# Performance work log

Hardware: AMD Instinct MI355X
Metric: run time of the kernel (lower is better)

Reference implementation:

```python
import jax, jax.numpy as jnp
import numpy as np

B, QS, KS, E, H = 2, 2048, 2048, 2048, 16
D = E // H  # head_dim = 128
EPS = 1e-6


def setup_inputs() -> dict:
    key = jax.random.key(0)
    ks = jax.random.split(key, 11)
    scale_in = 1.0 / np.sqrt(E)  # lecun_normal fan_in = E
    scale_out = 1.0 / np.sqrt(E)  # fan_in for out proj = H*D = E
    return {
        "q": jax.random.normal(ks[0], (B, QS, E), jnp.float32),
        "kv": jax.random.normal(ks[1], (B, KS, E), jnp.float32),
        "q_pos": jax.random.normal(ks[2], (B, QS, E), jnp.float32),
        "kv_pos": jax.random.normal(ks[3], (B, KS, E), jnp.float32),
        "mask": jax.random.bernoulli(ks[4], 0.5, (B, QS, KS)),
        "wq": jax.random.normal(ks[5], (E, H, D), jnp.float32) * scale_in,
        "wk": jax.random.normal(ks[6], (E, H, D), jnp.float32) * scale_in,
        "wv": jax.random.normal(ks[7], (E, H, D), jnp.float32) * scale_in,
        "q_ln_scale": jnp.ones((D,), jnp.float32),
        "k_ln_scale": jnp.ones((D,), jnp.float32),
        "wo": jax.random.normal(ks[8], (H, D, E), jnp.float32) * scale_out,
    }


def _layernorm_no_bias(x, scale):
    # flax LayerNorm over last axis, use_bias=False, epsilon=1e-6
    mu = jnp.mean(x, axis=-1, keepdims=True)
    var = jnp.mean(jnp.square(x - mu), axis=-1, keepdims=True)
    return (x - mu) * jax.lax.rsqrt(var + EPS) * scale


def reference(q, kv, q_pos, kv_pos, mask, wq, wk, wv, q_ln_scale, k_ln_scale, wo):
    dtype = q.dtype
    qi = q + q_pos          # [b, qs, e]
    ki = kv + kv_pos        # [b, ks, e]
    vi = kv
    # QKV projections (DenseGeneral, no bias) -> [b, s, h, d]
    qh = jnp.einsum('bqe,ehd->bqhd', qi, wq)
    kh = jnp.einsum('bke,ehd->bkhd', ki, wk)
    vh = jnp.einsum('bke,ehd->bkhd', vi, wv)
    # normalize_qk: LayerNorm (no bias) on query/key over head_dim
    qh = _layernorm_no_bias(qh, q_ln_scale)
    kh = _layernorm_no_bias(kh, k_ln_scale)
    # scaled dot-product with float32 logits
    qh = qh / jnp.sqrt(jnp.asarray(D, dtype))
    logits = jnp.einsum('bqhd,bkhd->bhqk', qh, kh,
                        preferred_element_type=jnp.float32)
    big_neg = jnp.finfo(jnp.float32).min
    logits = jnp.where(mask[:, None, :, :], logits, big_neg)
    attn = jax.nn.softmax(logits, axis=-1).astype(dtype)  # [b,h,q,k]
    out = jnp.einsum('bhqk,bkhd->bqhd', attn, vh)
    # output projection (DenseGeneral over (h,d), no bias)
    return jnp.einsum('bqhd,hde->bqe', out, wo)
```

## Files before the change

kernel.cpp:

```cpp
#include <hip/hip_runtime.h>
#include <hip/hip_bf16.h>


typedef __attribute__((ext_vector_type(8))) __bf16 bf16x8;
typedef __attribute__((ext_vector_type(4))) float f32x4;
typedef __attribute__((ext_vector_type(16))) float f32x16;
typedef __attribute__((ext_vector_type(8))) unsigned short ushort8;
typedef __attribute__((ext_vector_type(4))) unsigned short ushort4v;
typedef __attribute__((ext_vector_type(4))) unsigned uint4v;
typedef __attribute__((ext_vector_type(4))) float float4v;

#define MFMA16(a, b, c) __builtin_amdgcn_mfma_f32_16x16x32_bf16((a), (b), (c), 0, 0, 0)
#define MFMA32(a, b, c) __builtin_amdgcn_mfma_f32_32x32x16_bf16((a), (b), (c), 0, 0, 0)

__device__ __forceinline__ unsigned short f2bf(float f) {
  unsigned u = __builtin_bit_cast(unsigned, f);
  u += 0x7fffu + ((u >> 16) & 1u);
  return (unsigned short)(u >> 16);
}

__device__ __forceinline__ unsigned pkbf(float lo, float hi) {
  unsigned d;
  asm("v_cvt_pk_bf16_f32 %0, %1, %2" : "=v"(d) : "v"(lo), "v"(hi));
  return d;
}

__device__ __forceinline__ float max3f(float a, float b, float c) {
  float d;
  asm("v_max3_f32 %0, %1, %2, %3" : "=v"(d) : "v"(a), "v"(b), "v"(c));
  return d;
}

__device__ __forceinline__ float exp2a(float x) {
  float d;
  asm("v_exp_f32 %0, %1" : "=v"(d) : "v"(x));
  return d;
}

__device__ __forceinline__ void gload_lds16(const void* g, void* l) {
  __builtin_amdgcn_global_load_lds(
      (const __attribute__((address_space(1))) void*)g,
      (__attribute__((address_space(3))) void*)l, 16, 0, 0);
}

__global__ __launch_bounds__(256) void k_cvt(const float4v* __restrict__ x,
                                             const float4v* __restrict__ y,
                                             ushort4v* __restrict__ o, int n4) {
  int i = blockIdx.x * 256 + threadIdx.x;
  if (i >= n4) return;
  float4v a = x[i];
  if (y) { float4v b = y[i]; a = a + b; }
  ushort4v r;
  r[0] = f2bf(a[0]); r[1] = f2bf(a[1]); r[2] = f2bf(a[2]); r[3] = f2bf(a[3]);
  o[i] = r;
}

__global__ __launch_bounds__(256) void k_cvt2(const float4v* __restrict__ x,
                                              const float4v* __restrict__ y,
                                              ushort4v* __restrict__ oa,
                                              ushort4v* __restrict__ ob, int n4) {
  int i = blockIdx.x * 256 + threadIdx.x;
  if (i >= n4) return;
  float4v a = x[i];
  float4v s = a + y[i];
  ushort4v ra, rb;
  ra[0] = f2bf(s[0]); ra[1] = f2bf(s[1]); ra[2] = f2bf(s[2]); ra[3] = f2bf(s[3]);
  rb[0] = f2bf(a[0]); rb[1] = f2bf(a[1]); rb[2] = f2bf(a[2]); rb[3] = f2bf(a[3]);
  oa[i] = ra; ob[i] = rb;
}

__global__ __launch_bounds__(256) void k_tr(const float* __restrict__ s0, const float* __restrict__ s1,
                                            const float* __restrict__ s2, const float* __restrict__ s3,
                                            unsigned short* __restrict__ d0, unsigned short* __restrict__ d1,
                                            unsigned short* __restrict__ d2, unsigned short* __restrict__ d3) {
  __shared__ float t[32][33];
  const float* S; unsigned short* D;
  switch (blockIdx.z) {
    case 0: S = s0; D = d0; break;
    case 1: S = s1; D = d1; break;
    case 2: S = s2; D = d2; break;
    default: S = s3; D = d3; break;
  }
  int x = threadIdx.x & 31, y = threadIdx.x >> 5;
  int r0 = blockIdx.y * 32, c0 = blockIdx.x * 32;
#pragma unroll
  for (int i = 0; i < 4; ++i) t[y + 8 * i][x] = S[(size_t)(r0 + y + 8 * i) * 2048 + c0 + x];
  __syncthreads();
#pragma unroll
  for (int i = 0; i < 4; ++i)
    D[(size_t)(c0 + y + 8 * i) * 2048 + r0 + x] = f2bf(t[x][y + 8 * i]);
}

__global__ __launch_bounds__(256) void k_mask(const int* __restrict__ m,
                                              unsigned long long* __restrict__ out) {
  int i = blockIdx.x * 256 + threadIdx.x;
  unsigned long long b = __ballot(m[i] != 0);
  if ((threadIdx.x & 63) == 0) out[i >> 6] = b;
}

template <int MODE>
__global__ __launch_bounds__(256) void k_gemm(const unsigned short* __restrict__ A,
                                              const unsigned short* __restrict__ Bt,
                                              void* __restrict__ Cv,
                                              const float* __restrict__ lnsc) {
  constexpr int K = 2048;
  __shared__ __attribute__((aligned(16))) unsigned short sA[128 * 64];
  __shared__ __attribute__((aligned(16))) unsigned short sB[128 * 64];
  __shared__ float sSum[2][128];
  __shared__ float sSq[2][128];
  int tid = threadIdx.x;
  int lane = tid & 63, w = tid >> 6;
  int wr = w >> 1, wc = w & 1;
  int r15 = lane & 15, blk = lane >> 4;
  int n0 = blockIdx.x * 128, m0 = blockIdx.y * 128;
  const unsigned short* Abase = A + (size_t)m0 * K;
  const unsigned short* Bbase = Bt + (size_t)n0 * K;
  f32x4 acc[4][4] = {};

  for (int kt = 0; kt < K; kt += 64) {
#pragma unroll
    for (int i = 0; i < 4; ++i) {
      int c = i * 256 + tid;
      int row = c >> 3, cc = c & 7;
      gload_lds16(Abase + (size_t)row * K + kt + ((cc ^ (row & 7)) * 8), &sA[c * 8]);
    }
#pragma unroll
    for (int i = 0; i < 4; ++i) {
      int c = i * 256 + tid;
      int row = c >> 3, cc = c & 7;
      gload_lds16(Bbase + (size_t)row * K + kt + ((cc ^ (row & 7)) * 8), &sB[c * 8]);
    }
    __syncthreads();
#pragma unroll
    for (int kk = 0; kk < 2; ++kk) {
      bf16x8 av[4], bv[4];
#pragma unroll
      for (int i = 0; i < 4; ++i) {
        int row = wr * 64 + i * 16 + r15;
        av[i] = *(const bf16x8*)&sA[row * 64 + (((kk * 4 + blk) ^ (row & 7)) * 8)];
      }
#pragma unroll
      for (int j = 0; j < 4; ++j) {
        int row = wc * 64 + j * 16 + r15;
        bv[j] = *(const bf16x8*)&sB[row * 64 + (((kk * 4 + blk) ^ (row & 7)) * 8)];
      }
#pragma unroll
      for (int i = 0; i < 4; ++i)
#pragma unroll
        for (int j = 0; j < 4; ++j) acc[i][j] = MFMA16(av[i], bv[j], acc[i][j]);
    }
    __syncthreads();
  }

  if constexpr (MODE == 3) {
    float* C = (float*)Cv;
#pragma unroll
    for (int i = 0; i < 4; ++i)
#pragma unroll
      for (int r = 0; r < 4; ++r)
#pragma unroll
        for (int j = 0; j < 4; ++j) {
          int rowl = wr * 64 + i * 16 + blk * 4 + r;
          int coll = wc * 64 + j * 16 + r15;
          C[(size_t)(m0 + rowl) * 2048 + n0 + coll] = acc[i][j][r];
        }
    return;
  } else if constexpr (MODE == 4) {
    unsigned short* Vtp = (unsigned short*)Cv;
    int p15 = (r15 & 3) | ((r15 & 4) << 1) | ((r15 & 8) >> 1);
#pragma unroll
    for (int i = 0; i < 4; ++i)
#pragma unroll
      for (int r = 0; r < 4; ++r) {
        int rowg = m0 + wr * 64 + i * 16 + blk * 4 + r;
        int h = rowg >> 7, d = rowg & 127;
#pragma unroll
        for (int j = 0; j < 4; ++j) {
          int col = n0 + wc * 64 + j * 16;
          int b = col >> 11, s16 = col & 2047;
          Vtp[(((size_t)(b * 16 + h) * 128 + d) * 2048) + s16 + p15] = f2bf(acc[i][j][r]);
        }
      }
    return;
  } else {
    if constexpr (MODE == 1 || MODE == 2) {
#pragma unroll
      for (int i = 0; i < 4; ++i)
#pragma unroll
        for (int r = 0; r < 4; ++r) {
          float sm = 0.f, sq = 0.f;
#pragma unroll
          for (int j = 0; j < 4; ++j) { float v = acc[i][j][r]; sm += v; sq += v * v; }
          sm += __shfl_xor(sm, 1); sq += __shfl_xor(sq, 1);
          sm += __shfl_xor(sm, 2); sq += __shfl_xor(sq, 2);
          sm += __shfl_xor(sm, 4); sq += __shfl_xor(sq, 4);
          sm += __shfl_xor(sm, 8); sq += __shfl_xor(sq, 8);
          if (r15 == 0) {
            int rowl = wr * 64 + i * 16 + blk * 4 + r;
            sSum[wc][rowl] = sm; sSq[wc][rowl] = sq;
          }
        }
      __syncthreads();
    }
    unsigned short* Hout = (unsigned short*)Cv;
    int h = blockIdx.x;
#pragma unroll
    for (int i = 0; i < 4; ++i)
#pragma unroll
      for (int r = 0; r < 4; ++r) {
        int rowl = wr * 64 + i * 16 + blk * 4 + r;
        float mean = 0.f, rstd = 1.f;
        if constexpr (MODE == 1 || MODE == 2) {
          float sm = sSum[0][rowl] + sSum[1][rowl];
          float sq = sSq[0][rowl] + sSq[1][rowl];
          mean = sm * 0.0078125f;
          float var = sq * 0.0078125f - mean * mean;
          rstd = rsqrtf(var + 1e-6f);
        }
        int rowg = m0 + rowl;
        int b = rowg >> 11, s = rowg & 2047;
        unsigned short* orow = Hout + (((size_t)b * 16 + h) * 2048 + s) * 128;
#pragma unroll
        for (int j = 0; j < 4; ++j) {
          int d = wc * 64 + j * 16 + r15;
          float v = acc[i][j][r];
          if constexpr (MODE == 1)
            v = (v - mean) * rstd * lnsc[d] * (0.08838834764831845f * 1.4426950408889634f);
          if constexpr (MODE == 2) v = (v - mean) * rstd * lnsc[d];
          orow[d] = f2bf(v);
        }
      }
  }
}

__global__ __launch_bounds__(256, 2) void k_attn(const unsigned short* __restrict__ Qh,
                                                 const unsigned short* __restrict__ Kh,
                                                 const unsigned short* __restrict__ Vtp,
                                                 const unsigned* __restrict__ maskb,
                                                 unsigned short* __restrict__ O) {
  __shared__ __attribute__((aligned(16))) char smem[65536];
  int tid = threadIdx.x, w = tid >> 6;
  int lane = tid & 63;
  int q31 = lane & 31, hi = lane >> 5;
  int bh = blockIdx.y, b = bh >> 4, h = bh & 15;
  int qb = blockIdx.x * 128;
  size_t base = (size_t)bh * (2048 * 128);
  int qrow = qb + w * 32 + q31;

  bf16x8 qf[8];
  {
    const unsigned short* qp = Qh + base + (size_t)qrow * 128 + hi * 8;
#pragma unroll
    for (int wd = 0; wd < 8; ++wd) qf[wd] = *(const bf16x8*)(qp + wd * 16);
  }
  const unsigned* mrow = maskb + ((size_t)b * 2048 + qrow) * 64;

  const unsigned short* kgp[4];
  const unsigned short* vgp[4];
#pragma unroll
  for (int i = 0; i < 4; ++i) {
    int c = i * 256 + tid;
    int rr = c >> 4, cc = c & 15;
    kgp[i] = Kh + base + (size_t)rr * 128 + ((cc ^ (rr & 15)) * 8);
    int d = c >> 3, c8 = c & 7;
    vgp[i] = Vtp + base + (size_t)d * 2048 + ((c8 ^ (d & 7)) * 8);
  }

  f32x16 o[4] = {};
  float mv = -1e30f, ls = 0.f;

#pragma unroll
  for (int i = 0; i < 4; ++i) {
    int c = i * 256 + tid;
    gload_lds16(kgp[i], smem + c * 16);
    gload_lds16(vgp[i], smem + 16384 + c * 16);
  }

  int cur = 0;
  for (int kc = 0; kc < 2048; kc += 64) {
    if (kc + 64 < 2048) {
      char* nb = smem + ((cur ^ 1) << 15);
#pragma unroll
      for (int i = 0; i < 4; ++i) {
        int c = i * 256 + tid;
        gload_lds16(kgp[i] + (size_t)(kc + 64) * 128, nb + c * 16);
        gload_lds16(vgp[i] + (kc + 64), nb + 16384 + c * 16);
      }
      asm volatile("s_waitcnt vmcnt(8)" ::: "memory");
    } else {
      asm volatile("s_waitcnt vmcnt(0)" ::: "memory");
    }
    __builtin_amdgcn_s_barrier();
    __builtin_amdgcn_sched_barrier(0);
    const unsigned short* sK = (const unsigned short*)(smem + (cur << 15));
    const unsigned short* sV = (const unsigned short*)(smem + (cur << 15) + 16384);

    unsigned mw0 = mrow[kc >> 5] >> (4 * hi);
    unsigned mw1 = mrow[(kc >> 5) + 1] >> (4 * hi);

    f32x16 st0 = {}, st1 = {};
    __builtin_amdgcn_s_setprio(1);
#pragma unroll
    for (int wd = 0; wd < 8; ++wd) {
      int ck = ((2 * wd + hi) ^ (q31 & 15)) * 8;
      bf16x8 k0 = *(const bf16x8*)&sK[q31 * 128 + ck];
      bf16x8 k1 = *(const bf16x8*)&sK[(32 + q31) * 128 + ck];
      st0 = MFMA32(k0, qf[wd], st0);
      st1 = MFMA32(k1, qf[wd], st1);
    }
    __builtin_amdgcn_s_setprio(0);

    float pvv[32];
#pragma unroll
    for (int r = 0; r < 16; ++r) {
      int bit = (r & 3) + 8 * (r >> 2);
      pvv[r] = ((mw0 >> bit) & 1u) ? st0[r] : -1e30f;
      pvv[16 + r] = ((mw1 >> bit) & 1u) ? st1[r] : -1e30f;
    }
    float c0 = max3f(pvv[0], pvv[1], pvv[2]);
    float c1 = max3f(pvv[3], pvv[4], pvv[5]);
    float c2 = max3f(pvv[6], pvv[7], pvv[8]);
    float c3 = max3f(pvv[9], pvv[10], pvv[11]);
    float c4 = max3f(pvv[12], pvv[13], pvv[14]);
    float c5 = max3f(pvv[15], pvv[16], pvv[17]);
    float c6 = max3f(pvv[18], pvv[19], pvv[20]);
    float c7 = max3f(pvv[21], pvv[22], pvv[23]);
    float c8 = max3f(pvv[24], pvv[25], pvv[26]);
    float c9 = max3f(pvv[27], pvv[28], pvv[29]);
    float ca = fmaxf(pvv[30], pvv[31]);
    float t0 = max3f(c0, c1, c2);
    float t1 = max3f(c3, c4, c5);
    float t2 = max3f(c6, c7, c8);
    float t3 = max3f(c9, ca, t0);
    float cmax = max3f(t1, t2, t3);
    cmax = fmaxf(cmax, __shfl_xor(cmax, 32));

    if (!__all(cmax - mv <= 11.5f)) {
      float mnew = fmaxf(mv, cmax);
      float fac = exp2a(mv - mnew);
      ls *= fac;
      float fr[16];
#pragma unroll
      for (int r = 0; r < 16; ++r) fr[r] = __shfl(fac, (r & 3) + 8 * (r >> 2) + 4 * hi);
#pragma unroll
      for (int dt = 0; dt < 4; ++dt)
#pragma unroll
        for (int r = 0; r < 16; ++r) o[dt][r] *= fr[r];
      mv = mnew;
    }

#pragma unroll
    for (int t = 0; t < 32; ++t) pvv[t] = exp2a(pvv[t] - mv);
    {
      float s0 = 0.f, s1 = 0.f, s2 = 0.f, s3 = 0.f;
#pragma unroll
      for (int t = 0; t < 8; ++t) {
        s0 += pvv[t]; s1 += pvv[8 + t]; s2 += pvv[16 + t]; s3 += pvv[24 + t];
      }
      ls += (s0 + s1) + (s2 + s3);
    }

    bf16x8 pa[4];
#pragma unroll
    for (int kw = 0; kw < 4; ++kw) {
      uint4v pw;
#pragma unroll
      for (int m = 0; m < 4; ++m) pw[m] = pkbf(pvv[8 * kw + 2 * m], pvv[8 * kw + 2 * m + 1]);
      pa[kw] = __builtin_bit_cast(bf16x8, pw);
    }

    __builtin_amdgcn_s_setprio(1);
#pragma unroll
    for (int dt = 0; dt < 4; ++dt) {
      int vrow = dt * 32 + q31;
#pragma unroll
      for (int kw = 0; kw < 4; ++kw) {
        int cv = ((2 * kw + hi) ^ (q31 & 7)) * 8;
        bf16x8 vf = *(const bf16x8*)&sV[vrow * 64 + cv];
        o[dt] = MFMA32(pa[kw], vf, o[dt]);
      }
    }
    __builtin_amdgcn_s_setprio(0);
    asm volatile("s_waitcnt lgkmcnt(0)" ::: "memory");
    __builtin_amdgcn_s_barrier();
    cur ^= 1;
  }

  ls += __shfl_xor(ls, 32);
  float inv = 1.f / ls;
  float ir[16];
#pragma unroll
  for (int r = 0; r < 16; ++r) ir[r] = __shfl(inv, (r & 3) + 8 * (r >> 2) + 4 * hi);

  float* sO = (float*)smem;
#pragma unroll
  for (int pass = 0; pass < 2; ++pass) {
    __syncthreads();
    if ((w >> 1) == pass) {
      int wl = w & 1;
#pragma unroll
      for (int dt = 0; dt < 4; ++dt)
#pragma unroll
        for (int r = 0; r < 16; ++r) {
          int qrl = wl * 32 + (r & 3) + 8 * (r >> 2) + 4 * hi;
          sO[qrl * 132 + dt * 32 + q31] = o[dt][r] * ir[r];
        }
    }
    __syncthreads();
    {
      int row = tid >> 2, d0 = (tid & 3) * 32;
      int grow = qb + pass * 64 + row;
      unsigned short* op = O + (size_t)(b * 2048 + grow) * 2048 + h * 128 + d0;
#pragma unroll
      for (int g = 0; g < 4; ++g) {
        ushort8 pk;
#pragma unroll
        for (int e = 0; e < 8; ++e) pk[e] = f2bf(sO[row * 132 + d0 + g * 8 + e]);
        *(ushort8*)(op + g * 8) = pk;
      }
    }
  }
}

extern "C" void kernel_launch(void* const* d_in, const int* in_sizes, int n_in,
                              void* d_out, int out_size, void* d_ws, size_t ws_size,
                              hipStream_t stream) {
  const float* q      = (const float*)d_in[0];
  const float* kv     = (const float*)d_in[1];
  const float* q_pos  = (const float*)d_in[2];
  const float* kv_pos = (const float*)d_in[3];
  const int*   mask   = (const int*)d_in[4];
  const float* wq     = (const float*)d_in[5];
  const float* wk     = (const float*)d_in[6];
  const float* wv     = (const float*)d_in[7];
  const float* qls    = (const float*)d_in[8];
  const float* kls    = (const float*)d_in[9];
  const float* wo     = (const float*)d_in[10];

  char* ws = (char*)d_ws;
  const size_t SZ_ACT = (size_t)4096 * 2048 * 2;
  const size_t SZ_W   = (size_t)2048 * 2048 * 2;
  unsigned short* a_q = (unsigned short*)(ws);
  unsigned short* a_k = (unsigned short*)(ws + SZ_ACT);
  unsigned short* a_v = (unsigned short*)(ws + 2 * SZ_ACT);
  unsigned short* Qh  = (unsigned short*)(ws + 3 * SZ_ACT);
  unsigned short* Kh  = (unsigned short*)(ws + 4 * SZ_ACT);
  unsigned short* wqt = (unsigned short*)(ws + 6 * SZ_ACT);
  unsigned short* wkt = (unsigned short*)(ws + 6 * SZ_ACT + SZ_W);
  unsigned short* wvt = (unsigned short*)(ws + 6 * SZ_ACT + 2 * SZ_W);
  unsigned short* wot = (unsigned short*)(ws + 6 * SZ_ACT + 3 * SZ_W);
  unsigned*       mkb = (unsigned*)(ws + 6 * SZ_ACT + 4 * SZ_W);
  unsigned short* Ob  = a_q;
  unsigned short* Vtr = (unsigned short*)(ws + 5 * SZ_ACT);

  const size_t NEED = 6 * SZ_ACT + 4 * SZ_W + (size_t)2 * 2048 * 64 * 4;
  if (ws_size < NEED) return;

  k_cvt<<<8192, 256, 0, stream>>>((const float4v*)q, (const float4v*)q_pos, (ushort4v*)a_q, 2097152);
  k_cvt2<<<8192, 256, 0, stream>>>((const float4v*)kv, (const float4v*)kv_pos,
                                   (ushort4v*)a_k, (ushort4v*)a_v, 2097152);
  k_tr<<<dim3(64, 64, 4), 256, 0, stream>>>(wq, wk, wv, wo, wqt, wkt, wvt, wot);
  k_mask<<<32768, 256, 0, stream>>>(mask, (unsigned long long*)mkb);

  k_gemm<1><<<dim3(16, 32), 256, 0, stream>>>(a_q, wqt, Qh, qls);
  k_gemm<2><<<dim3(16, 32), 256, 0, stream>>>(a_k, wkt, Kh, kls);
  k_gemm<4><<<dim3(32, 16), 256, 0, stream>>>(wvt, a_v, Vtr, nullptr);

  k_attn<<<dim3(16, 32), 256, 0, stream>>>(Qh, Kh, Vtr, mkb, Ob);

  k_gemm<3><<<dim3(16, 32), 256, 0, stream>>>(Ob, wot, d_out, nullptr);
}
```

Baseline: 342.8 us.

## Use 256x128 triple-buffered 512-thread GEMM tiles and simplify attention loop sync

The projection GEMMs move to a 512-thread kernel with 256x128 output tiles and a three-stage asynchronous global-to-LDS pipeline, with hoisted load pointers and a four-way partial-sum reduction for the fused LayerNorm. The aim is to hide global load latency and raise data reuse per block. The attention loop drops its explicit vmcnt wait and barrier before compute and uses a full __syncthreads at the end of each iteration, plus one after the prologue. That sync change may reduce how well the K/V prefetch overlaps with compute. The GEMM uses 144KB of LDS per block, which limits occupancy to one block per CU and gives the launch about one block per CU.

```diff
diff --git a/kernel.cpp b/kernel.cpp
--- a/kernel.cpp
+++ b/kernel.cpp
@@ -99,134 +99,158 @@
 }
 
 template <int MODE>
-__global__ __launch_bounds__(256) void k_gemm(const unsigned short* __restrict__ A,
-                                              const unsigned short* __restrict__ Bt,
-                                              void* __restrict__ Cv,
-                                              const float* __restrict__ lnsc) {
+__global__ __launch_bounds__(512, 2) void k_gemm8(const unsigned short* __restrict__ A,
+                                                  const unsigned short* __restrict__ Bt,
+                                                  void* __restrict__ Cv,
+                                                  const float* __restrict__ lnsc) {
   constexpr int K = 2048;
-  __shared__ __attribute__((aligned(16))) unsigned short sA[128 * 64];
-  __shared__ __attribute__((aligned(16))) unsigned short sB[128 * 64];
-  __shared__ float sSum[2][128];
-  __shared__ float sSq[2][128];
+  constexpr int NT = 32;
+  constexpr int BUF = 49152;
+  __shared__ __attribute__((aligned(16))) char smem[3 * BUF];
   int tid = threadIdx.x;
   int lane = tid & 63, w = tid >> 6;
-  int wr = w >> 1, wc = w & 1;
+  int wr = w >> 2, wc = w & 3;
   int r15 = lane & 15, blk = lane >> 4;
-  int n0 = blockIdx.x * 128, m0 = blockIdx.y * 128;
+  int n0 = blockIdx.x * 128, m0 = blockIdx.y * 256;
   const unsigned short* Abase = A + (size_t)m0 * K;
   const unsigned short* Bbase = Bt + (size_t)n0 * K;
-  f32x4 acc[4][4] = {};
-
-  for (int kt = 0; kt < K; kt += 64) {
-#pragma unroll
-    for (int i = 0; i < 4; ++i) {
-      int c = i * 256 + tid;
-      int row = c >> 3, cc = c & 7;
-      gload_lds16(Abase + (size_t)row * K + kt + ((cc ^ (row & 7)) * 8), &sA[c * 8]);
-    }
-#pragma unroll
-    for (int i = 0; i < 4; ++i) {
-      int c = i * 256 + tid;
-      int row = c >> 3, cc = c & 7;
-      gload_lds16(Bbase + (size_t)row * K + kt + ((cc ^ (row & 7)) * 8), &sB[c * 8]);
-    }
-    __syncthreads();
+  f32x4 acc[8][2] = {};
+
+  const unsigned short* ag[4]; int al[4];
+  const unsigned short* bg[2]; int bl[2];
+#pragma unroll
+  for (int i = 0; i < 4; ++i) {
+    int c = i * 512 + tid;
+    int row = c >> 3, cc = c & 7;
+    ag[i] = Abase + (size_t)row * K + ((cc ^ (row & 7)) * 8);
+    al[i] = c * 16;
+  }
+#pragma unroll
+  for (int i = 0; i < 2; ++i) {
+    int c = i * 512 + tid;
+    int row = c >> 3, cc = c & 7;
+    bg[i] = Bbase + (size_t)row * K + ((cc ^ (row & 7)) * 8);
+    bl[i] = 32768 + c * 16;
+  }
+
+  auto stage = [&](int t) {
+    char* buf = smem + (t % 3) * BUF;
+    int kt = t * 64;
+#pragma unroll
+    for (int i = 0; i < 4; ++i) gload_lds16(ag[i] + kt, buf + al[i]);
+#pragma unroll
+    for (int i = 0; i < 2; ++i) gload_lds16(bg[i] + kt, buf + bl[i]);
+  };
+
+  stage(0);
+  stage(1);
+
+  for (int t = 0; t < NT; ++t) {
+    if (t + 2 < NT) {
+      stage(t + 2);
+      asm volatile("s_waitcnt vmcnt(6)" ::: "memory");
+    } else {
+      asm volatile("s_waitcnt vmcnt(0)" ::: "memory");
+    }
+    __builtin_amdgcn_s_barrier();
+    __builtin_amdgcn_sched_barrier(0);
+    const unsigned short* sA = (const unsigned short*)(smem + (t % 3) * BUF);
+    const unsigned short* sB = (const unsigned short*)(smem + (t % 3) * BUF + 32768);
 #pragma unroll
     for (int kk = 0; kk < 2; ++kk) {
-      bf16x8 av[4], bv[4];
-#pragma unroll
-      for (int i = 0; i < 4; ++i) {
-        int row = wr * 64 + i * 16 + r15;
+      bf16x8 av[8], bv[2];
+#pragma unroll
+      for (int i = 0; i < 8; ++i) {
+        int row = wr * 128 + i * 16 + r15;
         av[i] = *(const bf16x8*)&sA[row * 64 + (((kk * 4 + blk) ^ (row & 7)) * 8)];
       }
 #pragma unroll
-      for (int j = 0; j < 4; ++j) {
-        int row = wc * 64 + j * 16 + r15;
+      for (int j = 0; j < 2; ++j) {
+        int row = wc * 32 + j * 16 + r15;
         bv[j] = *(const bf16x8*)&sB[row * 64 + (((kk * 4 + blk) ^ (row & 7)) * 8)];
       }
 #pragma unroll
-      for (int i = 0; i < 4; ++i)
-#pragma unroll
-        for (int j = 0; j < 4; ++j) acc[i][j] = MFMA16(av[i], bv[j], acc[i][j]);
-    }
-    __syncthreads();
-  }
+      for (int i = 0; i < 8; ++i)
+#pragma unroll
+        for (int j = 0; j < 2; ++j) acc[i][j] = MFMA16(av[i], bv[j], acc[i][j]);
+    }
+    asm volatile("s_waitcnt lgkmcnt(0)" ::: "memory");
+    __builtin_amdgcn_s_barrier();
+  }
+  __syncthreads();
 
   if constexpr (MODE == 3) {
     float* C = (float*)Cv;
 #pragma unroll
-    for (int i = 0; i < 4; ++i)
-#pragma unroll
-      for (int r = 0; r < 4; ++r)
-#pragma unroll
-        for (int j = 0; j < 4; ++j) {
-          int rowl = wr * 64 + i * 16 + blk * 4 + r;
-          int coll = wc * 64 + j * 16 + r15;
+    for (int i = 0; i < 8; ++i)
+#pragma unroll
+      for (int r = 0; r < 4; ++r) {
+        int rowl = wr * 128 + i * 16 + blk * 4 + r;
+#pragma unroll
+        for (int j = 0; j < 2; ++j) {
+          int coll = wc * 32 + j * 16 + r15;
           C[(size_t)(m0 + rowl) * 2048 + n0 + coll] = acc[i][j][r];
         }
-    return;
+      }
   } else if constexpr (MODE == 4) {
     unsigned short* Vtp = (unsigned short*)Cv;
     int p15 = (r15 & 3) | ((r15 & 4) << 1) | ((r15 & 8) >> 1);
 #pragma unroll
-    for (int i = 0; i < 4; ++i)
+    for (int i = 0; i < 8; ++i)
 #pragma unroll
       for (int r = 0; r < 4; ++r) {
-        int rowg = m0 + wr * 64 + i * 16 + blk * 4 + r;
+        int rowg = m0 + wr * 128 + i * 16 + blk * 4 + r;
         int h = rowg >> 7, d = rowg & 127;
 #pragma unroll
-        for (int j = 0; j < 4; ++j) {
-          int col = n0 + wc * 64 + j * 16;
+        for (int j = 0; j < 2; ++j) {
+          int col = n0 + wc * 32 + j * 16;
           int b = col >> 11, s16 = col & 2047;
           Vtp[(((size_t)(b * 16 + h) * 128 + d) * 2048) + s16 + p15] = f2bf(acc[i][j][r]);
         }
       }
-    return;
   } else {
-    if constexpr (MODE == 1 || MODE == 2) {
-#pragma unroll
-      for (int i = 0; i < 4; ++i)
-#pragma unroll
-        for (int r = 0; r < 4; ++r) {
-          float sm = 0.f, sq = 0.f;
-#pragma unroll
-          for (int j = 0; j < 4; ++j) { float v = acc[i][j][r]; sm += v; sq += v * v; }
-          sm += __shfl_xor(sm, 1); sq += __shfl_xor(sq, 1);
-          sm += __shfl_xor(sm, 2); sq += __shfl_xor(sq, 2);
-          sm += __shfl_xor(sm, 4); sq += __shfl_xor(sq, 4);
-          sm += __shfl_xor(sm, 8); sq += __shfl_xor(sq, 8);
-          if (r15 == 0) {
-            int rowl = wr * 64 + i * 16 + blk * 4 + r;
-            sSum[wc][rowl] = sm; sSq[wc][rowl] = sq;
-          }
+    float* sSum = (float*)smem;
+    float* sSq  = (float*)smem + 1024;
+#pragma unroll
+    for (int i = 0; i < 8; ++i)
+#pragma unroll
+      for (int r = 0; r < 4; ++r) {
+        float v0 = acc[i][0][r], v1 = acc[i][1][r];
+        float sm = v0 + v1, sq = v0 * v0 + v1 * v1;
+        sm += __shfl_xor(sm, 1); sq += __shfl_xor(sq, 1);
+        sm += __shfl_xor(sm, 2); sq += __shfl_xor(sq, 2);
+        sm += __shfl_xor(sm, 4); sq += __shfl_xor(sq, 4);
+        sm += __shfl_xor(sm, 8); sq += __shfl_xor(sq, 8);
+        if (r15 == 0) {
+          int rowl = wr * 128 + i * 16 + blk * 4 + r;
+          sSum[wc * 256 + rowl] = sm;
+          sSq[wc * 256 + rowl] = sq;
         }
-      __syncthreads();
-    }
+      }
+    __syncthreads();
     unsigned short* Hout = (unsigned short*)Cv;
     int h = blockIdx.x;
 #pragma unroll
-    for (int i = 0; i < 4; ++i)
+    for (int i = 0; i < 8; ++i)
 #pragma unroll
       for (int r = 0; r < 4; ++r) {
-        int rowl = wr * 64 + i * 16 + blk * 4 + r;
-        float mean = 0.f, rstd = 1.f;
-        if constexpr (MODE == 1 || MODE == 2) {
-          float sm = sSum[0][rowl] + sSum[1][rowl];
-          float sq = sSq[0][rowl] + sSq[1][rowl];
-          mean = sm * 0.0078125f;
-          float var = sq * 0.0078125f - mean * mean;
-          rstd = rsqrtf(var + 1e-6f);
-        }
+        int rowl = wr * 128 + i * 16 + blk * 4 + r;
+        float sm = (sSum[rowl] + sSum[256 + rowl]) + (sSum[512 + rowl] + sSum[768 + rowl]);
+        float sq = (sSq[rowl] + sSq[256 + rowl]) + (sSq[512 + rowl] + sSq[768 + rowl]);
+        float mean = sm * 0.0078125f;
+        float var = sq * 0.0078125f - mean * mean;
+        float rstd = rsqrtf(var + 1e-6f);
         int rowg = m0 + rowl;
         int b = rowg >> 11, s = rowg & 2047;
         unsigned short* orow = Hout + (((size_t)b * 16 + h) * 2048 + s) * 128;
 #pragma unroll
-        for (int j = 0; j < 4; ++j) {
-          int d = wc * 64 + j * 16 + r15;
+        for (int j = 0; j < 2; ++j) {
+          int d = wc * 32 + j * 16 + r15;
           float v = acc[i][j][r];
           if constexpr (MODE == 1)
             v = (v - mean) * rstd * lnsc[d] * (0.08838834764831845f * 1.4426950408889634f);
-          if constexpr (MODE == 2) v = (v - mean) * rstd * lnsc[d];
+          else
+            v = (v - mean) * rstd * lnsc[d];
           orow[d] = f2bf(v);
         }
       }
@@ -275,6 +299,7 @@
     gload_lds16(kgp[i], smem + c * 16);
     gload_lds16(vgp[i], smem + 16384 + c * 16);
   }
+  __syncthreads();
 
   int cur = 0;
   for (int kc = 0; kc < 2048; kc += 64) {
@@ -286,12 +311,7 @@
         gload_lds16(kgp[i] + (size_t)(kc + 64) * 128, nb + c * 16);
         gload_lds16(vgp[i] + (kc + 64), nb + 16384 + c * 16);
       }
-      asm volatile("s_waitcnt vmcnt(8)" ::: "memory");
-    } else {
-      asm volatile("s_waitcnt vmcnt(0)" ::: "memory");
-    }
-    __builtin_amdgcn_s_barrier();
-    __builtin_amdgcn_sched_barrier(0);
+    }
     const unsigned short* sK = (const unsigned short*)(smem + (cur << 15));
     const unsigned short* sV = (const unsigned short*)(smem + (cur << 15) + 16384);
 
@@ -381,8 +401,7 @@
       }
     }
     __builtin_amdgcn_s_setprio(0);
-    asm volatile("s_waitcnt lgkmcnt(0)" ::: "memory");
-    __builtin_amdgcn_s_barrier();
+    __syncthreads();
     cur ^= 1;
   }
 
@@ -462,11 +481,11 @@
   k_tr<<<dim3(64, 64, 4), 256, 0, stream>>>(wq, wk, wv, wo, wqt, wkt, wvt, wot);
   k_mask<<<32768, 256, 0, stream>>>(mask, (unsigned long long*)mkb);
 
-  k_gemm<1><<<dim3(16, 32), 256, 0, stream>>>(a_q, wqt, Qh, qls);
-  k_gemm<2><<<dim3(16, 32), 256, 0, stream>>>(a_k, wkt, Kh, kls);
-  k_gemm<4><<<dim3(32, 16), 256, 0, stream>>>(wvt, a_v, Vtr, nullptr);
+  k_gemm8<1><<<dim3(16, 16), 512, 0, stream>>>(a_q, wqt, Qh, qls);
+  k_gemm8<2><<<dim3(16, 16), 512, 0, stream>>>(a_k, wkt, Kh, kls);
+  k_gemm8<4><<<dim3(32, 8), 512, 0, stream>>>(wvt, a_v, Vtr, nullptr);
 
   k_attn<<<dim3(16, 32), 256, 0, stream>>>(Qh, Kh, Vtr, mkb, Ob);
 
-  k_gemm<3><<<dim3(16, 32), 256, 0, stream>>>(Ob, wot, d_out, nullptr);
-}
+  k_gemm8<3><<<dim3(16, 16), 512, 0, stream>>>(Ob, wot, d_out, nullptr);
+}
```

Measured after the change: 326.1 us. -4.9%, faster.
